# Kernel tuning notes

Measured on AMD Instinct MI355X. Metric: run time of the kernel, lower is better.

## Reference

```python
import jax, jax.numpy as jnp
import numpy as np

B, C, D_MODEL, N_HEADS = 2, 2048, 1024, 16


def rotary_matrix(context_length: int, d: int) -> jnp.ndarray:
    """Faithful vectorization of get_rotary_matrix: theta = 10000^(-2*(i-1)/d)."""
    half = d // 2
    i = jnp.arange(half, dtype=jnp.float32)
    theta = 10000.0 ** (-2.0 * (i - 1.0) / d)          # note the (i-1), as in source
    m = jnp.arange(context_length, dtype=jnp.float32)
    ang = m[:, None] * theta                            # [C, d/2]
    c, s = jnp.cos(ang), jnp.sin(ang)
    ev = 2 * jnp.arange(half)
    od = ev + 1
    R = jnp.zeros((context_length, d, d), jnp.float32)
    R = R.at[:, ev, ev].set(c)
    R = R.at[:, ev, od].set(-s)
    R = R.at[:, od, ev].set(s)
    R = R.at[:, od, od].set(c)
    return R


def setup_inputs() -> dict:
    key = jax.random.key(0)
    k1, k2, k3, k4 = jax.random.split(key, 4)
    x = jax.random.normal(k1, (B, C, D_MODEL), dtype=jnp.float32)
    w_qkv = jax.random.normal(k2, (3 * D_MODEL, D_MODEL), dtype=jnp.float32) * 0.02
    w_out = jax.random.normal(k3, (D_MODEL, D_MODEL), dtype=jnp.float32) * 0.02
    b_out = jax.random.normal(k4, (D_MODEL,), dtype=jnp.float32) * 0.02
    return {"x": x, "w_qkv": w_qkv, "w_out": w_out, "b_out": b_out}


def reference(x, w_qkv, w_out, b_out):
    b, c, d = x.shape
    h = N_HEADS
    dh = d // h
    qkv = x @ w_qkv.T                                   # [B,C,3D]
    q, k, v = jnp.split(qkv, 3, axis=-1)
    # [B,C,D] -> [B,H,C,dh]
    q = q.reshape(b, c, h, dh).transpose(0, 2, 1, 3)
    k = k.reshape(b, c, h, dh).transpose(0, 2, 1, 3)
    v = v.reshape(b, c, h, dh).transpose(0, 2, 1, 3)
    R = rotary_matrix(c, dh)                            # [C,dh,dh]
    q_rot = jnp.einsum('bhci,cij->bhcj', q, R)
    k_rot = jnp.einsum('bhci,cij->bhcj', k, R)
    scale = jnp.sqrt(jnp.float32(dh))
    # exact math of the source: exp with no max subtraction, separate num/den
    attn_num = jnp.exp(jnp.einsum('bhqd,bhkd->bhqk', q_rot, k_rot) / scale)
    attn_den = jnp.exp(jnp.einsum('bhqd,bhkd->bhqk', q, k) / scale)
    attn_den = jnp.sum(attn_den, axis=-1, keepdims=True)
    attn = attn_num / attn_den
    causal = jnp.tril(jnp.ones((c, c), jnp.float32))[None, None]
    attn = jnp.where(causal == 0, 0.0, attn)
    y = jnp.einsum('bhqk,bhkd->bhqd', attn, v)
    y = y.transpose(0, 2, 1, 3).reshape(b, c, d)
    return y @ w_out.T + b_out
```

## Files before the change

### kernel.cpp

```cpp
#include <hip/hip_runtime.h>
#include <math.h>
#include <stdint.h>

#define BB 2
#define CC 2048
#define DD 1024
#define HH 16
#define DHH 64
#define HALF 32

typedef __attribute__((ext_vector_type(8))) short bf16x8;
typedef __attribute__((ext_vector_type(4))) float f32x4;
typedef unsigned int u32;

#define EXPC 0.1803368801f

__device__ __forceinline__ ushort f2bf(float f) {
    uint32_t u = __builtin_bit_cast(uint32_t, f);
    u = (u + 0x7FFFu + ((u >> 16) & 1u)) >> 16;
    return (ushort)u;
}

__device__ __forceinline__ void gload16(const void* g, void* lds) {
    __builtin_amdgcn_global_load_lds(
        (const u32 __attribute__((address_space(1)))*)g,
        (u32 __attribute__((address_space(3)))*)lds, 16, 0, 0);
}

__global__ __launch_bounds__(256) void cast3_k(const float* __restrict__ x,
                                               const float* __restrict__ wq,
                                               const float* __restrict__ wo,
                                               ushort* __restrict__ xb,
                                               ushort* __restrict__ wqb,
                                               ushort* __restrict__ wob) {
    int id = blockIdx.x * 256 + threadIdx.x;
    const float* s;
    ushort* d;
    int off;
    if (id < 524288)       { s = x;  d = xb;  off = id; }
    else if (id < 917504)  { s = wq; d = wqb; off = id - 524288; }
    else                   { s = wo; d = wob; off = id - 917504; }
    float4 a = *reinterpret_cast<const float4*>(s + (size_t)off * 8);
    float4 b = *reinterpret_cast<const float4*>(s + (size_t)off * 8 + 4);
    bf16x8 o;
    o[0] = (short)f2bf(a.x); o[1] = (short)f2bf(a.y);
    o[2] = (short)f2bf(a.z); o[3] = (short)f2bf(a.w);
    o[4] = (short)f2bf(b.x); o[5] = (short)f2bf(b.y);
    o[6] = (short)f2bf(b.z); o[7] = (short)f2bf(b.w);
    *reinterpret_cast<bf16x8*>(d + (size_t)off * 8) = o;
}

__global__ __launch_bounds__(256) void rope_table_k(float* __restrict__ ct, float* __restrict__ st) {
    int idx = blockIdx.x * 256 + threadIdx.x;
    if (idx >= CC * HALF) return;
    int m = idx >> 5;
    int t = idx & 31;
    double theta_d = pow(10000.0, -2.0 * ((double)t - 1.0) / 64.0);
    float theta = (float)theta_d;
    float ang = (float)m * theta;
    ct[idx] = cosf(ang);
    st[idx] = sinf(ang);
}

__global__ __launch_bounds__(256) void qkv_gemm_mfma_k(const ushort* __restrict__ xb,
                                                       const ushort* __restrict__ wqb,
                                                       const float* __restrict__ ct,
                                                       const float* __restrict__ st,
                                                       ushort* __restrict__ q,
                                                       ushort* __restrict__ k,
                                                       ushort* __restrict__ qr,
                                                       ushort* __restrict__ kr,
                                                       ushort* __restrict__ vT3) {
    __shared__ ushort Al[128 * 64];
    __shared__ ushort Bl[128 * 64];
    const int tid = threadIdx.x;
    const int w = tid >> 6, l = tid & 63;
    const int l15 = l & 15, lg = l >> 4;
    const int wr = w >> 1, wc = w & 1;
    const int m0 = blockIdx.x * 128, n0 = blockIdx.y * 128;
    const int lrow = l >> 3, lch = l & 7;

    f32x4 acc[4][4];
#pragma unroll
    for (int i = 0; i < 4; i++)
#pragma unroll
        for (int j = 0; j < 4; j++) acc[i][j] = (f32x4){0.f, 0.f, 0.f, 0.f};

    for (int k0 = 0; k0 < 1024; k0 += 64) {
        __syncthreads();
#pragma unroll
        for (int c = 0; c < 4; c++) {
            int row = w * 32 + c * 8 + lrow;
            int gch = (lch ^ (row & 7)) * 8;
            gload16(xb + (size_t)(m0 + row) * 1024 + k0 + gch, &Al[(w * 32 + c * 8) * 64]);
            gload16(wqb + (size_t)(n0 + row) * 1024 + k0 + gch, &Bl[(w * 32 + c * 8) * 64]);
        }
        __syncthreads();
#pragma unroll
        for (int kk = 0; kk < 2; kk++) {
            bf16x8 a[4], b[4];
#pragma unroll
            for (int mt = 0; mt < 4; mt++) {
                int row = wr * 64 + mt * 16 + l15;
                a[mt] = *reinterpret_cast<const bf16x8*>(&Al[row * 64 + ((kk * 4 + lg) ^ (row & 7)) * 8]);
            }
#pragma unroll
            for (int nt = 0; nt < 4; nt++) {
                int row = wc * 64 + nt * 16 + l15;
                b[nt] = *reinterpret_cast<const bf16x8*>(&Bl[row * 64 + ((kk * 4 + lg) ^ (row & 7)) * 8]);
            }
#pragma unroll
            for (int mt = 0; mt < 4; mt++)
#pragma unroll
                for (int nt = 0; nt < 4; nt++)
                    acc[mt][nt] = __builtin_amdgcn_mfma_f32_16x16x32_bf16(a[mt], b[nt], acc[mt][nt], 0, 0, 0);
        }
    }
#pragma unroll
    for (int mt = 0; mt < 4; mt++)
#pragma unroll
        for (int nt = 0; nt < 4; nt++) {
            int n = n0 + wc * 64 + nt * 16 + l15;
            int part = n >> 10;
            int d = n & 1023;
            int h = d >> 6, dd = d & 63;
            int mbase = m0 + wr * 64 + mt * 16 + lg * 4;
            int bb = mbase >> 11, cpos = mbase & 2047;
            if (part == 2) {
                int kt = cpos >> 6, kcol = cpos & 63;
                ushort4 pk;
                pk.x = f2bf(acc[mt][nt][0]); pk.y = f2bf(acc[mt][nt][1]);
                pk.z = f2bf(acc[mt][nt][2]); pk.w = f2bf(acc[mt][nt][3]);
                size_t off = ((((size_t)(bb * HH + h)) * 32 + kt) * 64 + dd) * 64 + kcol;
                *reinterpret_cast<ushort4*>(vT3 + off) = pk;
            } else {
                ushort* dstu = (part == 0) ? q : k;
                ushort* dstr = (part == 0) ? qr : kr;
                const float sgn = (dd & 1) ? -1.f : 1.f;
                const int t = dd >> 1;
#pragma unroll
                for (int r = 0; r < 4; r++) {
                    float val = acc[mt][nt][r];
                    float par = __shfl_xor(val, 1, 64);
                    float c = ct[(cpos + r) * 32 + t];
                    float s = st[(cpos + r) * 32 + t];
                    float rot = val * c + sgn * par * s;
                    size_t base = (((size_t)bb * HH + h) * CC + (cpos + r)) * DHH + dd;
                    dstu[base] = f2bf(val);
                    dstr[base] = f2bf(rot);
                }
            }
        }
}

__global__ __launch_bounds__(256) void den_k(const ushort* __restrict__ qg,
                                             const ushort* __restrict__ kg,
                                             float* __restrict__ deng) {
    __shared__ ushort Kd[2][128 * 64];
    const int tid = threadIdx.x;
    const int w = tid >> 6, l = tid & 63;
    const int l15 = l & 15, lg = l >> 4;
    const int lrow = l >> 3, lch = l & 7;
    const int bh = blockIdx.y;
    const int q0 = blockIdx.x * 128;
    const ushort* qb = qg + (size_t)bh * CC * DHH;
    const ushort* kb = kg + (size_t)bh * CC * DHH;

    bf16x8 qf[2][2];
#pragma unroll
    for (int mt = 0; mt < 2; mt++)
#pragma unroll
        for (int kk = 0; kk < 2; kk++) {
            int row = q0 + w * 32 + mt * 16 + l15;
            qf[mt][kk] = *reinterpret_cast<const bf16x8*>(qb + (size_t)row * DHH + kk * 32 + lg * 8);
        }

    float dacc[2] = {0.f, 0.f};

#define DSTAGE(KT, BUF)                                                                     \
    {                                                                                       \
        const int sk0 = (KT) * 128;                                                         \
        _Pragma("unroll")                                                                   \
        for (int c = 0; c < 4; c++) {                                                       \
            int row = w * 32 + c * 8 + lrow;                                                \
            int gch = (lch ^ (row & 7)) * 8;                                                \
            gload16(kb + (size_t)(sk0 + row) * DHH + gch, &Kd[BUF][(w * 32 + c * 8) * 64]); \
        }                                                                                   \
    }

    DSTAGE(0, 0);
    __syncthreads();
    int cur = 0;

    for (int kt = 0; kt < 16; kt++) {
        if (kt < 15) DSTAGE(kt + 1, cur ^ 1);
#pragma unroll
        for (int nt = 0; nt < 8; nt++) {
            bf16x8 ka[2];
#pragma unroll
            for (int kk = 0; kk < 2; kk++) {
                int krow = nt * 16 + l15;
                ka[kk] = *reinterpret_cast<const bf16x8*>(
                    &Kd[cur][krow * 64 + ((kk * 4 + lg) ^ (krow & 7)) * 8]);
            }
#pragma unroll
            for (int mt = 0; mt < 2; mt++) {
                f32x4 s = (f32x4){0.f, 0.f, 0.f, 0.f};
                s = __builtin_amdgcn_mfma_f32_16x16x32_bf16(ka[0], qf[mt][0], s, 0, 0, 0);
                s = __builtin_amdgcn_mfma_f32_16x16x32_bf16(ka[1], qf[mt][1], s, 0, 0, 0);
#pragma unroll
                for (int r = 0; r < 4; r++)
                    dacc[mt] += __builtin_amdgcn_exp2f(s[r] * EXPC);
            }
        }
        __syncthreads();
        cur ^= 1;
    }
#pragma unroll
    for (int mt = 0; mt < 2; mt++) {
        float d = dacc[mt];
        d += __shfl_xor(d, 16, 64);
        d += __shfl_xor(d, 32, 64);
        if (lg == 0)
            deng[(size_t)bh * CC + q0 + w * 32 + mt * 16 + l15] = d;
    }
#undef DSTAGE
}

__global__ __launch_bounds__(256, 5) void attn_mfma_k(const ushort* __restrict__ vT3,
                                                      const ushort* __restrict__ qrg,
                                                      const ushort* __restrict__ krg,
                                                      const float* __restrict__ deng,
                                                      ushort* __restrict__ y) {
    __shared__ ushort Krl[2][64 * 64];
    __shared__ ushort Pl[4][16 * 64];

    const int tid = threadIdx.x;
    const int w = tid >> 6, l = tid & 63;
    const int l15 = l & 15, lg = l >> 4;
    const int lrow = l >> 3, lch = l & 7;

    const int bid = blockIdx.x;
    const int xcd = bid & 7;
    const int idx = bid >> 3;
    const int sub = idx >> 5;
    const int xt = idx & 31;
    const int tile = (sub & 1) ? (31 - xt) : xt;
    const int bh = xcd * 4 + sub;
    const int q0 = tile * 64;

    const ushort* qrb = qrg + (size_t)bh * CC * DHH;
    const ushort* krb = krg + (size_t)bh * CC * DHH;
    const ushort* vtb = vT3 + (size_t)bh * 32 * 64 * 64;

    bf16x8 qrf[2];
#pragma unroll
    for (int kk = 0; kk < 2; kk++) {
        int row = q0 + w * 16 + l15;
        qrf[kk] = *reinterpret_cast<const bf16x8*>(qrb + (size_t)row * DHH + kk * 32 + lg * 8);
    }

    f32x4 yacc[4];
#pragma unroll
    for (int nt = 0; nt < 4; nt++) yacc[nt] = (f32x4){0.f, 0.f, 0.f, 0.f};

#define STAGE(KT, BUF)                                                                         \
    {                                                                                          \
        const int sk0 = (KT) * 64;                                                             \
        _Pragma("unroll")                                                                      \
        for (int c = 0; c < 2; c++) {                                                          \
            int row = w * 16 + c * 8 + lrow;                                                   \
            int gch = (lch ^ (row & 7)) * 8;                                                   \
            gload16(krb + (size_t)(sk0 + row) * DHH + gch, &Krl[BUF][(w * 16 + c * 8) * 64]);  \
        }                                                                                      \
    }

    STAGE(0, 0);
    __syncthreads();
    int cur = 0;

    for (int kt = 0; kt <= tile; kt++) {
        bf16x8 vf[4][2];
        const ushort* vt0 = vtb + (size_t)kt * 64 * 64;
#pragma unroll
        for (int nt2 = 0; nt2 < 4; nt2++)
#pragma unroll
            for (int kk2 = 0; kk2 < 2; kk2++)
                vf[nt2][kk2] = *reinterpret_cast<const bf16x8*>(
                    vt0 + (nt2 * 16 + l15) * 64 + kk2 * 32 + lg * 8);

        if (kt < tile) STAGE(kt + 1, cur ^ 1);

        const bool diag = (kt == tile);
        const int qrow = q0 + w * 16 + l15;
#pragma unroll
        for (int nt = 0; nt < 4; nt++) {
            f32x4 s = (f32x4){0.f, 0.f, 0.f, 0.f};
#pragma unroll
            for (int kk = 0; kk < 2; kk++) {
                int krow = nt * 16 + l15;
                bf16x8 ka = *reinterpret_cast<const bf16x8*>(
                    &Krl[cur][krow * 64 + ((kk * 4 + lg) ^ (krow & 7)) * 8]);
                s = __builtin_amdgcn_mfma_f32_16x16x32_bf16(ka, qrf[kk], s, 0, 0, 0);
            }
            float pe[4];
#pragma unroll
            for (int r = 0; r < 4; r++)
                pe[r] = __builtin_amdgcn_exp2f(s[r] * EXPC);
            if (diag) {
#pragma unroll
                for (int r = 0; r < 4; r++) {
                    int key = kt * 64 + nt * 16 + lg * 4 + r;
                    pe[r] = (key <= qrow) ? pe[r] : 0.f;
                }
            }
            u32 pk0, pk1;
            asm("v_cvt_pk_bf16_f32 %0, %1, %2" : "=v"(pk0) : "v"(pe[0]), "v"(pe[1]));
            asm("v_cvt_pk_bf16_f32 %0, %1, %2" : "=v"(pk1) : "v"(pe[2]), "v"(pe[3]));
            int swzc = (nt * 2 + (lg >> 1)) ^ (l15 & 7);
            uint2 pr; pr.x = pk0; pr.y = pk1;
            *reinterpret_cast<uint2*>(&Pl[w][l15 * 64 + swzc * 8 + (lg & 1) * 4]) = pr;
        }
        bf16x8 pa[2];
#pragma unroll
        for (int kk2 = 0; kk2 < 2; kk2++) {
            int rc = (kk2 * 4 + lg) ^ (l15 & 7);
            pa[kk2] = *reinterpret_cast<const bf16x8*>(&Pl[w][l15 * 64 + rc * 8]);
        }
#pragma unroll
        for (int nt2 = 0; nt2 < 4; nt2++)
#pragma unroll
            for (int kk2 = 0; kk2 < 2; kk2++)
                yacc[nt2] = __builtin_amdgcn_mfma_f32_16x16x32_bf16(pa[kk2], vf[nt2][kk2],
                                                                    yacc[nt2], 0, 0, 0);
        __syncthreads();
        cur ^= 1;
    }

    const int b = bh >> 4, h = bh & 15;
#pragma unroll
    for (int r = 0; r < 4; r++) {
        int row = q0 + w * 16 + lg * 4 + r;
        float inv = 1.f / deng[(size_t)bh * CC + row];
#pragma unroll
        for (int nt2 = 0; nt2 < 4; nt2++)
            y[((size_t)b * CC + row) * DD + h * DHH + nt2 * 16 + l15] = f2bf(yacc[nt2][r] * inv);
    }
#undef STAGE
}

__global__ __launch_bounds__(256) void out_proj_mfma_k(const ushort* __restrict__ yb,
                                                       const ushort* __restrict__ wob,
                                                       const float* __restrict__ bias,
                                                       float* __restrict__ out) {
    __shared__ ushort Al[128 * 64];
    __shared__ ushort Bl[128 * 64];
    const int tid = threadIdx.x;
    const int w = tid >> 6, l = tid & 63;
    const int l15 = l & 15, lg = l >> 4;
    const int wr = w >> 1, wc = w & 1;
    const int m0 = blockIdx.x * 128, n0 = blockIdx.y * 128;
    const int lrow = l >> 3, lch = l & 7;

    f32x4 acc[4][4];
#pragma unroll
    for (int i = 0; i < 4; i++)
#pragma unroll
        for (int j = 0; j < 4; j++) acc[i][j] = (f32x4){0.f, 0.f, 0.f, 0.f};

    for (int k0 = 0; k0 < 1024; k0 += 64) {
        __syncthreads();
#pragma unroll
        for (int c = 0; c < 4; c++) {
            int row = w * 32 + c * 8 + lrow;
            int gch = (lch ^ (row & 7)) * 8;
            gload16(yb + (size_t)(m0 + row) * 1024 + k0 + gch, &Al[(w * 32 + c * 8) * 64]);
            gload16(wob + (size_t)(n0 + row) * 1024 + k0 + gch, &Bl[(w * 32 + c * 8) * 64]);
        }
        __syncthreads();
#pragma unroll
        for (int kk = 0; kk < 2; kk++) {
            bf16x8 a[4], b[4];
#pragma unroll
            for (int mt = 0; mt < 4; mt++) {
                int row = wr * 64 + mt * 16 + l15;
                a[mt] = *reinterpret_cast<const bf16x8*>(&Al[row * 64 + ((kk * 4 + lg) ^ (row & 7)) * 8]);
            }
#pragma unroll
            for (int nt = 0; nt < 4; nt++) {
                int row = wc * 64 + nt * 16 + l15;
                b[nt] = *reinterpret_cast<const bf16x8*>(&Bl[row * 64 + ((kk * 4 + lg) ^ (row & 7)) * 8]);
            }
#pragma unroll
            for (int mt = 0; mt < 4; mt++)
#pragma unroll
                for (int nt = 0; nt < 4; nt++)
                    acc[mt][nt] = __builtin_amdgcn_mfma_f32_16x16x32_bf16(a[mt], b[nt], acc[mt][nt], 0, 0, 0);
        }
    }
#pragma unroll
    for (int mt = 0; mt < 4; mt++)
#pragma unroll
        for (int nt = 0; nt < 4; nt++) {
            int n = n0 + wc * 64 + nt * 16 + l15;
            float bv = bias[n];
#pragma unroll
            for (int r = 0; r < 4; r++) {
                int m = m0 + wr * 64 + mt * 16 + lg * 4 + r;
                out[(size_t)m * 1024 + n] = acc[mt][nt][r] + bv;
            }
        }
}

extern "C" void kernel_launch(void* const* d_in, const int* in_sizes, int n_in,
                              void* d_out, int out_size, void* d_ws, size_t ws_size,
                              hipStream_t stream) {
    (void)in_sizes; (void)n_in; (void)out_size; (void)ws_size;
    const float* x     = (const float*)d_in[0];
    const float* w_qkv = (const float*)d_in[1];
    const float* w_out = (const float*)d_in[2];
    const float* b_out = (const float*)d_in[3];
    float* out = (float*)d_out;

    char* p = (char*)d_ws;
    float* ct = (float*)p;  p += (size_t)CC * HALF * 4;
    float* st = (float*)p;  p += (size_t)CC * HALF * 4;
    ushort* xb  = (ushort*)p; p += (size_t)4096 * 1024 * 2;
    ushort* wqb = (ushort*)p; p += (size_t)3072 * 1024 * 2;
    ushort* wob = (ushort*)p; p += (size_t)1024 * 1024 * 2;
    const size_t TEN = (size_t)BB * HH * CC * DHH;
    ushort* qb = (ushort*)p; p += TEN * 2;
    ushort* kb = (ushort*)p; p += TEN * 2;
    ushort* vT = (ushort*)p; p += TEN * 2;
    ushort* qr = (ushort*)p; p += TEN * 2;
    ushort* kr = (ushort*)p; p += TEN * 2;
    ushort* yb = (ushort*)p; p += (size_t)4096 * 1024 * 2;
    float* den = (float*)p;  p += (size_t)32 * CC * 4;

    cast3_k<<<dim3(4096), dim3(256), 0, stream>>>(x, w_qkv, w_out, xb, wqb, wob);
    rope_table_k<<<dim3((CC * HALF) / 256), dim3(256), 0, stream>>>(ct, st);
    qkv_gemm_mfma_k<<<dim3(32, 24), dim3(256), 0, stream>>>(xb, wqb, ct, st, qb, kb, qr, kr, vT);
    den_k<<<dim3(16, 32), dim3(256), 0, stream>>>(qb, kb, den);
    attn_mfma_k<<<dim3(1024), dim3(256), 0, stream>>>(vT, qr, kr, den, yb);
    out_proj_mfma_k<<<dim3(32, 8), dim3(256), 0, stream>>>(yb, wob, b_out, out);
}
```

Before: 181.0 us.

## Pair causal query tiles per block to share K/V staging; shrink den tiles

The attention kernel now gives each block two query tiles (tp and 31-tp) of the same head. Each staged K tile and each V fragment load serves both tiles, and every block does the same amount of causal work. The grid is halved to 512 blocks, and launch bounds drop to 2 blocks per SM to leave room for the doubled accumulators. The denominator kernel moves to 64-row query tiles with twice as many blocks, trading K reuse for more parallelism; the lower occupancy in attention is a risk.

```diff
diff --git a/kernel.cpp b/kernel.cpp
--- a/kernel.cpp
+++ b/kernel.cpp
@@ -162,18 +162,16 @@
     const int l15 = l & 15, lg = l >> 4;
     const int lrow = l >> 3, lch = l & 7;
     const int bh = blockIdx.y;
-    const int q0 = blockIdx.x * 128;
+    const int q0 = blockIdx.x * 64;
     const ushort* qb = qg + (size_t)bh * CC * DHH;
     const ushort* kb = kg + (size_t)bh * CC * DHH;
 
-    bf16x8 qf[2][2];
-#pragma unroll
-    for (int mt = 0; mt < 2; mt++)
-#pragma unroll
-        for (int kk = 0; kk < 2; kk++) {
-            int row = q0 + w * 32 + mt * 16 + l15;
-            qf[mt][kk] = *reinterpret_cast<const bf16x8*>(qb + (size_t)row * DHH + kk * 32 + lg * 8);
-        }
+    bf16x8 qf[2];
+#pragma unroll
+    for (int kk = 0; kk < 2; kk++) {
+        int row = q0 + w * 16 + l15;
+        qf[kk] = *reinterpret_cast<const bf16x8*>(qb + (size_t)row * DHH + kk * 32 + lg * 8);
+    }
 
     float dacc[2] = {0.f, 0.f};
 
@@ -196,38 +194,30 @@
         if (kt < 15) DSTAGE(kt + 1, cur ^ 1);
 #pragma unroll
         for (int nt = 0; nt < 8; nt++) {
-            bf16x8 ka[2];
+            f32x4 s = (f32x4){0.f, 0.f, 0.f, 0.f};
 #pragma unroll
             for (int kk = 0; kk < 2; kk++) {
                 int krow = nt * 16 + l15;
-                ka[kk] = *reinterpret_cast<const bf16x8*>(
+                bf16x8 ka = *reinterpret_cast<const bf16x8*>(
                     &Kd[cur][krow * 64 + ((kk * 4 + lg) ^ (krow & 7)) * 8]);
-            }
-#pragma unroll
-            for (int mt = 0; mt < 2; mt++) {
-                f32x4 s = (f32x4){0.f, 0.f, 0.f, 0.f};
-                s = __builtin_amdgcn_mfma_f32_16x16x32_bf16(ka[0], qf[mt][0], s, 0, 0, 0);
-                s = __builtin_amdgcn_mfma_f32_16x16x32_bf16(ka[1], qf[mt][1], s, 0, 0, 0);
-#pragma unroll
-                for (int r = 0; r < 4; r++)
-                    dacc[mt] += __builtin_amdgcn_exp2f(s[r] * EXPC);
-            }
+                s = __builtin_amdgcn_mfma_f32_16x16x32_bf16(ka, qf[kk], s, 0, 0, 0);
+            }
+#pragma unroll
+            for (int r = 0; r < 4; r++)
+                dacc[nt & 1] += __builtin_amdgcn_exp2f(s[r] * EXPC);
         }
         __syncthreads();
         cur ^= 1;
     }
-#pragma unroll
-    for (int mt = 0; mt < 2; mt++) {
-        float d = dacc[mt];
-        d += __shfl_xor(d, 16, 64);
-        d += __shfl_xor(d, 32, 64);
-        if (lg == 0)
-            deng[(size_t)bh * CC + q0 + w * 32 + mt * 16 + l15] = d;
-    }
+    float d = dacc[0] + dacc[1];
+    d += __shfl_xor(d, 16, 64);
+    d += __shfl_xor(d, 32, 64);
+    if (lg == 0)
+        deng[(size_t)bh * CC + q0 + w * 16 + l15] = d;
 #undef DSTAGE
 }
 
-__global__ __launch_bounds__(256, 5) void attn_mfma_k(const ushort* __restrict__ vT3,
+__global__ __launch_bounds__(256, 2) void attn_pair_k(const ushort* __restrict__ vT3,
                                                       const ushort* __restrict__ qrg,
                                                       const ushort* __restrict__ krg,
                                                       const float* __restrict__ deng,
@@ -243,26 +233,30 @@
     const int bid = blockIdx.x;
     const int xcd = bid & 7;
     const int idx = bid >> 3;
-    const int sub = idx >> 5;
-    const int xt = idx & 31;
-    const int tile = (sub & 1) ? (31 - xt) : xt;
+    const int sub = idx & 3;
+    const int tp = idx >> 2;
     const int bh = xcd * 4 + sub;
-    const int q0 = tile * 64;
+    const int q0a = tp * 64;
+    const int NB = 31 - tp;
+    const int q0b = NB * 64;
 
     const ushort* qrb = qrg + (size_t)bh * CC * DHH;
     const ushort* krb = krg + (size_t)bh * CC * DHH;
     const ushort* vtb = vT3 + (size_t)bh * 32 * 64 * 64;
 
-    bf16x8 qrf[2];
+    bf16x8 qrfA[2], qrfB[2];
 #pragma unroll
     for (int kk = 0; kk < 2; kk++) {
-        int row = q0 + w * 16 + l15;
-        qrf[kk] = *reinterpret_cast<const bf16x8*>(qrb + (size_t)row * DHH + kk * 32 + lg * 8);
-    }
-
-    f32x4 yacc[4];
-#pragma unroll
-    for (int nt = 0; nt < 4; nt++) yacc[nt] = (f32x4){0.f, 0.f, 0.f, 0.f};
+        qrfA[kk] = *reinterpret_cast<const bf16x8*>(qrb + (size_t)(q0a + w * 16 + l15) * DHH + kk * 32 + lg * 8);
+        qrfB[kk] = *reinterpret_cast<const bf16x8*>(qrb + (size_t)(q0b + w * 16 + l15) * DHH + kk * 32 + lg * 8);
+    }
+
+    f32x4 yaccA[4], yaccB[4];
+#pragma unroll
+    for (int nt = 0; nt < 4; nt++) {
+        yaccA[nt] = (f32x4){0.f, 0.f, 0.f, 0.f};
+        yaccB[nt] = (f32x4){0.f, 0.f, 0.f, 0.f};
+    }
 
 #define STAGE(KT, BUF)                                                                         \
     {                                                                                          \
@@ -275,11 +269,57 @@
         }                                                                                      \
     }
 
+#define NUMPV(Q0, QRF, YACC, LASTKT)                                                           \
+    {                                                                                          \
+        const bool diag = (kt == (LASTKT));                                                    \
+        const int qrow = (Q0) + w * 16 + l15;                                                  \
+        _Pragma("unroll")                                                                      \
+        for (int nt = 0; nt < 4; nt++) {                                                       \
+            f32x4 s = (f32x4){0.f, 0.f, 0.f, 0.f};                                             \
+            _Pragma("unroll")                                                                  \
+            for (int kk = 0; kk < 2; kk++) {                                                   \
+                int krow = nt * 16 + l15;                                                      \
+                bf16x8 ka = *reinterpret_cast<const bf16x8*>(                                  \
+                    &Krl[cur][krow * 64 + ((kk * 4 + lg) ^ (krow & 7)) * 8]);                  \
+                s = __builtin_amdgcn_mfma_f32_16x16x32_bf16(ka, (QRF)[kk], s, 0, 0, 0);        \
+            }                                                                                  \
+            float pe[4];                                                                       \
+            _Pragma("unroll")                                                                  \
+            for (int r = 0; r < 4; r++)                                                        \
+                pe[r] = __builtin_amdgcn_exp2f(s[r] * EXPC);                                   \
+            if (diag) {                                                                        \
+                _Pragma("unroll")                                                              \
+                for (int r = 0; r < 4; r++) {                                                  \
+                    int key = kt * 64 + nt * 16 + lg * 4 + r;                                  \
+                    pe[r] = (key <= qrow) ? pe[r] : 0.f;                                       \
+                }                                                                              \
+            }                                                                                  \
+            u32 pk0, pk1;                                                                      \
+            asm("v_cvt_pk_bf16_f32 %0, %1, %2" : "=v"(pk0) : "v"(pe[0]), "v"(pe[1]));          \
+            asm("v_cvt_pk_bf16_f32 %0, %1, %2" : "=v"(pk1) : "v"(pe[2]), "v"(pe[3]));          \
+            int swzc = (nt * 2 + (lg >> 1)) ^ (l15 & 7);                                       \
+            uint2 pr; pr.x = pk0; pr.y = pk1;                                                  \
+            *reinterpret_cast<uint2*>(&Pl[w][l15 * 64 + swzc * 8 + (lg & 1) * 4]) = pr;        \
+        }                                                                                      \
+        bf16x8 pa[2];                                                                          \
+        _Pragma("unroll")                                                                      \
+        for (int kk2 = 0; kk2 < 2; kk2++) {                                                    \
+            int rc = (kk2 * 4 + lg) ^ (l15 & 7);                                               \
+            pa[kk2] = *reinterpret_cast<const bf16x8*>(&Pl[w][l15 * 64 + rc * 8]);             \
+        }                                                                                      \
+        _Pragma("unroll")                                                                      \
+        for (int nt2 = 0; nt2 < 4; nt2++)                                                      \
+            _Pragma("unroll")                                                                  \
+            for (int kk2 = 0; kk2 < 2; kk2++)                                                  \
+                (YACC)[nt2] = __builtin_amdgcn_mfma_f32_16x16x32_bf16(pa[kk2], vf[nt2][kk2],   \
+                                                                      (YACC)[nt2], 0, 0, 0);   \
+    }
+
     STAGE(0, 0);
     __syncthreads();
     int cur = 0;
 
-    for (int kt = 0; kt <= tile; kt++) {
+    for (int kt = 0; kt <= NB; kt++) {
         bf16x8 vf[4][2];
         const ushort* vt0 = vtb + (size_t)kt * 64 * 64;
 #pragma unroll
@@ -289,50 +329,11 @@
                 vf[nt2][kk2] = *reinterpret_cast<const bf16x8*>(
                     vt0 + (nt2 * 16 + l15) * 64 + kk2 * 32 + lg * 8);
 
-        if (kt < tile) STAGE(kt + 1, cur ^ 1);
-
-        const bool diag = (kt == tile);
-        const int qrow = q0 + w * 16 + l15;
-#pragma unroll
-        for (int nt = 0; nt < 4; nt++) {
-            f32x4 s = (f32x4){0.f, 0.f, 0.f, 0.f};
-#pragma unroll
-            for (int kk = 0; kk < 2; kk++) {
-                int krow = nt * 16 + l15;
-                bf16x8 ka = *reinterpret_cast<const bf16x8*>(
-                    &Krl[cur][krow * 64 + ((kk * 4 + lg) ^ (krow & 7)) * 8]);
-                s = __builtin_amdgcn_mfma_f32_16x16x32_bf16(ka, qrf[kk], s, 0, 0, 0);
-            }
-            float pe[4];
-#pragma unroll
-            for (int r = 0; r < 4; r++)
-                pe[r] = __builtin_amdgcn_exp2f(s[r] * EXPC);
-            if (diag) {
-#pragma unroll
-                for (int r = 0; r < 4; r++) {
-                    int key = kt * 64 + nt * 16 + lg * 4 + r;
-                    pe[r] = (key <= qrow) ? pe[r] : 0.f;
-                }
-            }
-            u32 pk0, pk1;
-            asm("v_cvt_pk_bf16_f32 %0, %1, %2" : "=v"(pk0) : "v"(pe[0]), "v"(pe[1]));
-            asm("v_cvt_pk_bf16_f32 %0, %1, %2" : "=v"(pk1) : "v"(pe[2]), "v"(pe[3]));
-            int swzc = (nt * 2 + (lg >> 1)) ^ (l15 & 7);
-            uint2 pr; pr.x = pk0; pr.y = pk1;
-            *reinterpret_cast<uint2*>(&Pl[w][l15 * 64 + swzc * 8 + (lg & 1) * 4]) = pr;
-        }
-        bf16x8 pa[2];
-#pragma unroll
-        for (int kk2 = 0; kk2 < 2; kk2++) {
-            int rc = (kk2 * 4 + lg) ^ (l15 & 7);
-            pa[kk2] = *reinterpret_cast<const bf16x8*>(&Pl[w][l15 * 64 + rc * 8]);
-        }
-#pragma unroll
-        for (int nt2 = 0; nt2 < 4; nt2++)
-#pragma unroll
-            for (int kk2 = 0; kk2 < 2; kk2++)
-                yacc[nt2] = __builtin_amdgcn_mfma_f32_16x16x32_bf16(pa[kk2], vf[nt2][kk2],
-                                                                    yacc[nt2], 0, 0, 0);
+        if (kt < NB) STAGE(kt + 1, cur ^ 1);
+
+        if (kt <= tp) NUMPV(q0a, qrfA, yaccA, tp);
+        NUMPV(q0b, qrfB, yaccB, NB);
+
         __syncthreads();
         cur ^= 1;
     }
@@ -340,13 +341,18 @@
     const int b = bh >> 4, h = bh & 15;
 #pragma unroll
     for (int r = 0; r < 4; r++) {
-        int row = q0 + w * 16 + lg * 4 + r;
-        float inv = 1.f / deng[(size_t)bh * CC + row];
-#pragma unroll
-        for (int nt2 = 0; nt2 < 4; nt2++)
-            y[((size_t)b * CC + row) * DD + h * DHH + nt2 * 16 + l15] = f2bf(yacc[nt2][r] * inv);
+        int rowA = q0a + w * 16 + lg * 4 + r;
+        int rowB = q0b + w * 16 + lg * 4 + r;
+        float invA = 1.f / deng[(size_t)bh * CC + rowA];
+        float invB = 1.f / deng[(size_t)bh * CC + rowB];
+#pragma unroll
+        for (int nt2 = 0; nt2 < 4; nt2++) {
+            y[((size_t)b * CC + rowA) * DD + h * DHH + nt2 * 16 + l15] = f2bf(yaccA[nt2][r] * invA);
+            y[((size_t)b * CC + rowB) * DD + h * DHH + nt2 * 16 + l15] = f2bf(yaccB[nt2][r] * invB);
+        }
     }
 #undef STAGE
+#undef NUMPV
 }
 
 __global__ __launch_bounds__(256) void out_proj_mfma_k(const ushort* __restrict__ yb,
@@ -440,7 +446,7 @@
     cast3_k<<<dim3(4096), dim3(256), 0, stream>>>(x, w_qkv, w_out, xb, wqb, wob);
     rope_table_k<<<dim3((CC * HALF) / 256), dim3(256), 0, stream>>>(ct, st);
     qkv_gemm_mfma_k<<<dim3(32, 24), dim3(256), 0, stream>>>(xb, wqb, ct, st, qb, kb, qr, kr, vT);
-    den_k<<<dim3(16, 32), dim3(256), 0, stream>>>(qb, kb, den);
-    attn_mfma_k<<<dim3(1024), dim3(256), 0, stream>>>(vT, qr, kr, den, yb);
+    den_k<<<dim3(32, 32), dim3(256), 0, stream>>>(qb, kb, den);
+    attn_pair_k<<<dim3(512), dim3(256), 0, stream>>>(vT, qr, kr, den, yb);
     out_proj_mfma_k<<<dim3(32, 8), dim3(256), 0, stream>>>(yb, wob, b_out, out);
 }
```

Result: faster. 176.1 us (-2.7%).

## Split denominator over key halves and pair causal tiles per attention block

Applied to the files above, without the earlier changes.

The denominator kernel now splits the key range into two halves across a third grid dimension, processing 64 query rows per block, and writes two partial sums that the attention kernel adds. The attention kernel pairs a short causal tile with its complementary long tile inside one block (two waves each, 32 rows per block half), so every block does roughly equal work and shares staged K loads. Waves on the short tile sit idle through the later iterations but still reach the barriers. Occupancy bound drops from 5 to 4 blocks.

```diff
diff --git a/kernel.cpp b/kernel.cpp
--- a/kernel.cpp
+++ b/kernel.cpp
@@ -162,18 +162,17 @@
     const int l15 = l & 15, lg = l >> 4;
     const int lrow = l >> 3, lch = l & 7;
     const int bh = blockIdx.y;
-    const int q0 = blockIdx.x * 128;
+    const int q0 = blockIdx.x * 64;
+    const int kh = blockIdx.z;
     const ushort* qb = qg + (size_t)bh * CC * DHH;
-    const ushort* kb = kg + (size_t)bh * CC * DHH;
-
-    bf16x8 qf[2][2];
-#pragma unroll
-    for (int mt = 0; mt < 2; mt++)
-#pragma unroll
-        for (int kk = 0; kk < 2; kk++) {
-            int row = q0 + w * 32 + mt * 16 + l15;
-            qf[mt][kk] = *reinterpret_cast<const bf16x8*>(qb + (size_t)row * DHH + kk * 32 + lg * 8);
-        }
+    const ushort* kb = kg + (size_t)bh * CC * DHH + (size_t)kh * 1024 * DHH;
+
+    bf16x8 qf[2];
+#pragma unroll
+    for (int kk = 0; kk < 2; kk++) {
+        int row = q0 + w * 16 + l15;
+        qf[kk] = *reinterpret_cast<const bf16x8*>(qb + (size_t)row * DHH + kk * 32 + lg * 8);
+    }
 
     float dacc[2] = {0.f, 0.f};
 
@@ -192,42 +191,34 @@
     __syncthreads();
     int cur = 0;
 
-    for (int kt = 0; kt < 16; kt++) {
-        if (kt < 15) DSTAGE(kt + 1, cur ^ 1);
+    for (int kt = 0; kt < 8; kt++) {
+        if (kt < 7) DSTAGE(kt + 1, cur ^ 1);
 #pragma unroll
         for (int nt = 0; nt < 8; nt++) {
-            bf16x8 ka[2];
+            f32x4 s = (f32x4){0.f, 0.f, 0.f, 0.f};
 #pragma unroll
             for (int kk = 0; kk < 2; kk++) {
                 int krow = nt * 16 + l15;
-                ka[kk] = *reinterpret_cast<const bf16x8*>(
+                bf16x8 ka = *reinterpret_cast<const bf16x8*>(
                     &Kd[cur][krow * 64 + ((kk * 4 + lg) ^ (krow & 7)) * 8]);
-            }
-#pragma unroll
-            for (int mt = 0; mt < 2; mt++) {
-                f32x4 s = (f32x4){0.f, 0.f, 0.f, 0.f};
-                s = __builtin_amdgcn_mfma_f32_16x16x32_bf16(ka[0], qf[mt][0], s, 0, 0, 0);
-                s = __builtin_amdgcn_mfma_f32_16x16x32_bf16(ka[1], qf[mt][1], s, 0, 0, 0);
-#pragma unroll
-                for (int r = 0; r < 4; r++)
-                    dacc[mt] += __builtin_amdgcn_exp2f(s[r] * EXPC);
-            }
+                s = __builtin_amdgcn_mfma_f32_16x16x32_bf16(ka, qf[kk], s, 0, 0, 0);
+            }
+#pragma unroll
+            for (int r = 0; r < 4; r++)
+                dacc[nt & 1] += __builtin_amdgcn_exp2f(s[r] * EXPC);
         }
         __syncthreads();
         cur ^= 1;
     }
-#pragma unroll
-    for (int mt = 0; mt < 2; mt++) {
-        float d = dacc[mt];
-        d += __shfl_xor(d, 16, 64);
-        d += __shfl_xor(d, 32, 64);
-        if (lg == 0)
-            deng[(size_t)bh * CC + q0 + w * 32 + mt * 16 + l15] = d;
-    }
+    float d = dacc[0] + dacc[1];
+    d += __shfl_xor(d, 16, 64);
+    d += __shfl_xor(d, 32, 64);
+    if (lg == 0)
+        deng[((size_t)kh * 32 + bh) * CC + q0 + w * 16 + l15] = d;
 #undef DSTAGE
 }
 
-__global__ __launch_bounds__(256, 5) void attn_mfma_k(const ushort* __restrict__ vT3,
+__global__ __launch_bounds__(256, 4) void attn_pair_k(const ushort* __restrict__ vT3,
                                                       const ushort* __restrict__ qrg,
                                                       const ushort* __restrict__ krg,
                                                       const float* __restrict__ deng,
@@ -243,11 +234,15 @@
     const int bid = blockIdx.x;
     const int xcd = bid & 7;
     const int idx = bid >> 3;
-    const int sub = idx >> 5;
-    const int xt = idx & 31;
-    const int tile = (sub & 1) ? (31 - xt) : xt;
+    const int sub = idx & 3;
+    const int rest = idx >> 2;
+    const int tp = rest >> 1;
+    const int h2 = rest & 1;
     const int bh = xcd * 4 + sub;
-    const int q0 = tile * 64;
+    const int NB = 31 - tp;
+
+    const int myTile = (w < 2) ? tp : NB;
+    const int qrow0 = myTile * 64 + h2 * 32 + (w & 1) * 16;
 
     const ushort* qrb = qrg + (size_t)bh * CC * DHH;
     const ushort* krb = krg + (size_t)bh * CC * DHH;
@@ -255,10 +250,9 @@
 
     bf16x8 qrf[2];
 #pragma unroll
-    for (int kk = 0; kk < 2; kk++) {
-        int row = q0 + w * 16 + l15;
-        qrf[kk] = *reinterpret_cast<const bf16x8*>(qrb + (size_t)row * DHH + kk * 32 + lg * 8);
-    }
+    for (int kk = 0; kk < 2; kk++)
+        qrf[kk] = *reinterpret_cast<const bf16x8*>(
+            qrb + (size_t)(qrow0 + l15) * DHH + kk * 32 + lg * 8);
 
     f32x4 yacc[4];
 #pragma unroll
@@ -279,60 +273,66 @@
     __syncthreads();
     int cur = 0;
 
-    for (int kt = 0; kt <= tile; kt++) {
+    for (int kt = 0; kt <= NB; kt++) {
+        const bool active = (kt <= myTile);
+
         bf16x8 vf[4][2];
-        const ushort* vt0 = vtb + (size_t)kt * 64 * 64;
-#pragma unroll
-        for (int nt2 = 0; nt2 < 4; nt2++)
-#pragma unroll
-            for (int kk2 = 0; kk2 < 2; kk2++)
-                vf[nt2][kk2] = *reinterpret_cast<const bf16x8*>(
-                    vt0 + (nt2 * 16 + l15) * 64 + kk2 * 32 + lg * 8);
-
-        if (kt < tile) STAGE(kt + 1, cur ^ 1);
-
-        const bool diag = (kt == tile);
-        const int qrow = q0 + w * 16 + l15;
-#pragma unroll
-        for (int nt = 0; nt < 4; nt++) {
-            f32x4 s = (f32x4){0.f, 0.f, 0.f, 0.f};
-#pragma unroll
-            for (int kk = 0; kk < 2; kk++) {
-                int krow = nt * 16 + l15;
-                bf16x8 ka = *reinterpret_cast<const bf16x8*>(
-                    &Krl[cur][krow * 64 + ((kk * 4 + lg) ^ (krow & 7)) * 8]);
-                s = __builtin_amdgcn_mfma_f32_16x16x32_bf16(ka, qrf[kk], s, 0, 0, 0);
-            }
-            float pe[4];
-#pragma unroll
-            for (int r = 0; r < 4; r++)
-                pe[r] = __builtin_amdgcn_exp2f(s[r] * EXPC);
-            if (diag) {
-#pragma unroll
-                for (int r = 0; r < 4; r++) {
-                    int key = kt * 64 + nt * 16 + lg * 4 + r;
-                    pe[r] = (key <= qrow) ? pe[r] : 0.f;
+        if (active) {
+            const ushort* vt0 = vtb + (size_t)kt * 64 * 64;
+#pragma unroll
+            for (int nt2 = 0; nt2 < 4; nt2++)
+#pragma unroll
+                for (int kk2 = 0; kk2 < 2; kk2++)
+                    vf[nt2][kk2] = *reinterpret_cast<const bf16x8*>(
+                        vt0 + (nt2 * 16 + l15) * 64 + kk2 * 32 + lg * 8);
+        }
+
+        if (kt < NB) STAGE(kt + 1, cur ^ 1);
+
+        if (active) {
+            const bool diag = (kt == myTile);
+            const int qrow = qrow0 + l15;
+#pragma unroll
+            for (int nt = 0; nt < 4; nt++) {
+                f32x4 s = (f32x4){0.f, 0.f, 0.f, 0.f};
+#pragma unroll
+                for (int kk = 0; kk < 2; kk++) {
+                    int krow = nt * 16 + l15;
+                    bf16x8 ka = *reinterpret_cast<const bf16x8*>(
+                        &Krl[cur][krow * 64 + ((kk * 4 + lg) ^ (krow & 7)) * 8]);
+                    s = __builtin_amdgcn_mfma_f32_16x16x32_bf16(ka, qrf[kk], s, 0, 0, 0);
                 }
-            }
-            u32 pk0, pk1;
-            asm("v_cvt_pk_bf16_f32 %0, %1, %2" : "=v"(pk0) : "v"(pe[0]), "v"(pe[1]));
-            asm("v_cvt_pk_bf16_f32 %0, %1, %2" : "=v"(pk1) : "v"(pe[2]), "v"(pe[3]));
-            int swzc = (nt * 2 + (lg >> 1)) ^ (l15 & 7);
-            uint2 pr; pr.x = pk0; pr.y = pk1;
-            *reinterpret_cast<uint2*>(&Pl[w][l15 * 64 + swzc * 8 + (lg & 1) * 4]) = pr;
-        }
-        bf16x8 pa[2];
-#pragma unroll
-        for (int kk2 = 0; kk2 < 2; kk2++) {
-            int rc = (kk2 * 4 + lg) ^ (l15 & 7);
-            pa[kk2] = *reinterpret_cast<const bf16x8*>(&Pl[w][l15 * 64 + rc * 8]);
-        }
-#pragma unroll
-        for (int nt2 = 0; nt2 < 4; nt2++)
-#pragma unroll
-            for (int kk2 = 0; kk2 < 2; kk2++)
-                yacc[nt2] = __builtin_amdgcn_mfma_f32_16x16x32_bf16(pa[kk2], vf[nt2][kk2],
-                                                                    yacc[nt2], 0, 0, 0);
+                float pe[4];
+#pragma unroll
+                for (int r = 0; r < 4; r++)
+                    pe[r] = __builtin_amdgcn_exp2f(s[r] * EXPC);
+                if (diag) {
+#pragma unroll
+                    for (int r = 0; r < 4; r++) {
+                        int key = kt * 64 + nt * 16 + lg * 4 + r;
+                        pe[r] = (key <= qrow) ? pe[r] : 0.f;
+                    }
+                }
+                u32 pk0, pk1;
+                asm("v_cvt_pk_bf16_f32 %0, %1, %2" : "=v"(pk0) : "v"(pe[0]), "v"(pe[1]));
+                asm("v_cvt_pk_bf16_f32 %0, %1, %2" : "=v"(pk1) : "v"(pe[2]), "v"(pe[3]));
+                int swzc = (nt * 2 + (lg >> 1)) ^ (l15 & 7);
+                uint2 pr; pr.x = pk0; pr.y = pk1;
+                *reinterpret_cast<uint2*>(&Pl[w][l15 * 64 + swzc * 8 + (lg & 1) * 4]) = pr;
+            }
+            bf16x8 pa[2];
+#pragma unroll
+            for (int kk2 = 0; kk2 < 2; kk2++) {
+                int rc = (kk2 * 4 + lg) ^ (l15 & 7);
+                pa[kk2] = *reinterpret_cast<const bf16x8*>(&Pl[w][l15 * 64 + rc * 8]);
+            }
+#pragma unroll
+            for (int nt2 = 0; nt2 < 4; nt2++)
+#pragma unroll
+                for (int kk2 = 0; kk2 < 2; kk2++)
+                    yacc[nt2] = __builtin_amdgcn_mfma_f32_16x16x32_bf16(pa[kk2], vf[nt2][kk2],
+                                                                        yacc[nt2], 0, 0, 0);
+        }
         __syncthreads();
         cur ^= 1;
     }
@@ -340,8 +340,9 @@
     const int b = bh >> 4, h = bh & 15;
 #pragma unroll
     for (int r = 0; r < 4; r++) {
-        int row = q0 + w * 16 + lg * 4 + r;
-        float inv = 1.f / deng[(size_t)bh * CC + row];
+        int row = qrow0 + lg * 4 + r;
+        float den = deng[(size_t)bh * CC + row] + deng[(size_t)(32 + bh) * CC + row];
+        float inv = 1.f / den;
 #pragma unroll
         for (int nt2 = 0; nt2 < 4; nt2++)
             y[((size_t)b * CC + row) * DD + h * DHH + nt2 * 16 + l15] = f2bf(yacc[nt2][r] * inv);
@@ -435,12 +436,12 @@
     ushort* qr = (ushort*)p; p += TEN * 2;
     ushort* kr = (ushort*)p; p += TEN * 2;
     ushort* yb = (ushort*)p; p += (size_t)4096 * 1024 * 2;
-    float* den = (float*)p;  p += (size_t)32 * CC * 4;
+    float* den = (float*)p;  p += (size_t)2 * 32 * CC * 4;
 
     cast3_k<<<dim3(4096), dim3(256), 0, stream>>>(x, w_qkv, w_out, xb, wqb, wob);
     rope_table_k<<<dim3((CC * HALF) / 256), dim3(256), 0, stream>>>(ct, st);
     qkv_gemm_mfma_k<<<dim3(32, 24), dim3(256), 0, stream>>>(xb, wqb, ct, st, qb, kb, qr, kr, vT);
-    den_k<<<dim3(16, 32), dim3(256), 0, stream>>>(qb, kb, den);
-    attn_mfma_k<<<dim3(1024), dim3(256), 0, stream>>>(vT, qr, kr, den, yb);
+    den_k<<<dim3(32, 32, 2), dim3(256), 0, stream>>>(qb, kb, den);
+    attn_pair_k<<<dim3(1024), dim3(256), 0, stream>>>(vT, qr, kr, den, yb);
     out_proj_mfma_k<<<dim3(32, 8), dim3(256), 0, stream>>>(yb, wob, b_out, out);
 }
```

Result: no change. 183.3 us (+1.3%).
